# Kernel tuning notes

Hardware: AMD Instinct MI355X
Metric: run time of the kernel (lower is better)

## Reference

```python
import jax, jax.numpy as jnp
import numpy as np

NBITS = 4
GROUP = 128
K = 4096   # in_features
N = 4096   # out_features
M = 4096   # flattened batch*seq tokens
EPS = 32 // NBITS  # elements per packed int32 = 8
MASK = (1 << NBITS) - 1  # unpack_mask = 15


def setup_inputs() -> dict:
    key = jax.random.key(0)
    k1, k2, k3, k4, k5 = jax.random.split(key, 5)
    x = jax.random.normal(k1, (M, K), dtype=jnp.float32)
    # raw 4-bit quantized weights, layout [K, N] (i.e. W_q.t() from the torch module)
    nib = jax.random.randint(k2, (K, N), 0, 1 << NBITS, dtype=jnp.int32)
    # pack EPS nibbles per int32 along K, matching pack(): element j gets shift j*NBITS
    nib = nib.reshape(K // EPS, EPS, N)
    shifts = (jnp.arange(EPS, dtype=jnp.int32) * NBITS)[None, :, None]
    parts = nib << shifts  # disjoint bit ranges
    W_q_packed = parts[:, 0]
    for j in range(1, EPS):
        W_q_packed = W_q_packed | parts[:, j]
    W_q_packed = W_q_packed.astype(jnp.int32)  # [K//EPS, N]
    # group-wise scales/zeros: [K//GROUP, N] (scales.view(N,-1).t() layout)
    scales = (jax.random.uniform(k3, (K // GROUP, N), dtype=jnp.float32) + 0.5) * 0.01
    zeros = jax.random.uniform(k4, (K // GROUP, N), dtype=jnp.float32) * MASK
    bias = jax.random.normal(k5, (N,), dtype=jnp.float32) * 0.1
    return {"x": x, "W_q_packed": W_q_packed, "scales": scales, "zeros": zeros, "bias": bias}


def reference(x, W_q_packed, scales, zeros, bias):
    # unpack: w[k, n] = (packed[k//EPS, n] >> ((k % EPS) * NBITS)) & MASK
    shifts = (jnp.arange(EPS, dtype=jnp.int32) * NBITS)[None, :, None]
    w = (W_q_packed[:, None, :] >> shifts) & MASK  # [K//EPS, EPS, N]
    w = w.reshape(K, N).astype(jnp.float32)
    # group-wise asymmetric dequant (W_group_mode == 3): W = (w - z) * s
    s = jnp.repeat(scales, GROUP, axis=0)  # [K, N]
    z = jnp.repeat(zeros, GROUP, axis=0)   # [K, N]
    W = (w - z) * s
    out = x @ W + bias  # [M, N]
    return out
```

## Files before the change

kernel.cpp:

```cpp
#include <hip/hip_runtime.h>
#include <stdint.h>


#define M_DIM 4096
#define N_DIM 4096
#define K_DIM 4096
#define NT (K_DIM / 64)

typedef __attribute__((ext_vector_type(8))) short short8;
typedef __attribute__((ext_vector_type(4))) float f32x4;

__device__ __forceinline__ unsigned short f2bf(float f) {
  uint32_t u = __builtin_bit_cast(uint32_t, f);
  u += 0x7fffu + ((u >> 16) & 1u);
  return (unsigned short)(u >> 16);
}

__global__ __launch_bounds__(256) void prep_kernel(const float* __restrict__ x,
                                                   unsigned short* __restrict__ xb,
                                                   const int* __restrict__ Wq,
                                                   const float* __restrict__ scales,
                                                   const float* __restrict__ zeros,
                                                   unsigned short* __restrict__ wt) {
  __shared__ uint4 Ts[32 * 64];
  const int tid = threadIdx.x;
  if (blockIdx.x < 2048) {
    const int total = (M_DIM * K_DIM) / 8;
    const float4* x4 = (const float4*)x;
    uint4* o8 = (uint4*)xb;
#pragma unroll
    for (int p = 0; p < 4; ++p) {
      int i = (p * 2048 + blockIdx.x) * 256 + tid;
      if (i < total) {
        float4 a = x4[2 * i], b = x4[2 * i + 1];
        uint4 o;
        o.x = (uint32_t)f2bf(a.x) | ((uint32_t)f2bf(a.y) << 16);
        o.y = (uint32_t)f2bf(a.z) | ((uint32_t)f2bf(a.w) << 16);
        o.z = (uint32_t)f2bf(b.x) | ((uint32_t)f2bf(b.y) << 16);
        o.w = (uint32_t)f2bf(b.z) | ((uint32_t)f2bf(b.w) << 16);
        o8[i] = o;
      }
    }
    return;
  }
  const int blk = blockIdx.x - 2048;
  const int n0 = (blk & 127) * 32;
  const int gk0 = (blk >> 7) * 64;

#pragma unroll
  for (int p = 0; p < 8; ++p) {
    int e = p * 256 + tid;
    int n_l = e & 31;
    int gk_l = e >> 5;
    int gk = gk0 + gk_l;
    int n = n0 + n_l;
    int g = gk >> 4;
    uint32_t q = (uint32_t)Wq[gk * N_DIM + n];
    float s = scales[g * N_DIM + n];
    float z = zeros[g * N_DIM + n];
    unsigned short b[8];
#pragma unroll
    for (int j = 0; j < 8; ++j) {
      float f = ((float)((q >> (4 * j)) & 15u) - z) * s;
      b[j] = f2bf(f);
    }
    uint4 cell;
    cell.x = (uint32_t)b[0] | ((uint32_t)b[1] << 16);
    cell.y = (uint32_t)b[2] | ((uint32_t)b[3] << 16);
    cell.z = (uint32_t)b[4] | ((uint32_t)b[5] << 16);
    cell.w = (uint32_t)b[6] | ((uint32_t)b[7] << 16);
    Ts[n_l * 64 + (gk_l ^ (n_l & 7))] = cell;
  }
  __syncthreads();
  uint4* dst = (uint4*)wt;
#pragma unroll
  for (int p = 0; p < 8; ++p) {
    int n_l = p * 4 + (tid >> 6);
    int gk_l = tid & 63;
    uint4 cell = Ts[n_l * 64 + (gk_l ^ (n_l & 7))];
    dst[(size_t)(n0 + n_l) * (K_DIM / 8) + (gk0 + gk_l)] = cell;
  }
}


#define STAGE4(DST, SRC)                                                         \
  {                                                                              \
    _Pragma("unroll") for (int j = 0; j < 4; ++j)                                \
        __builtin_amdgcn_global_load_lds(                                        \
            (const __attribute__((address_space(1))) void*)((SRC) +              \
                                                            (size_t)j * 64 * K_DIM), \
            (__attribute__((address_space(3))) void*)((DST) + tid + j * 512),    \
            16, 0, 0);                                                           \
  }

#define LOADA(QM)                                                                \
  {                                                                              \
    _Pragma("unroll") for (int mi = 0; mi < 4; ++mi) {                           \
      af[mi][0] = ASb[a_base + ((QM) * 4 + mi) * 128 + kx0];                     \
      af[mi][1] = ASb[a_base + ((QM) * 4 + mi) * 128 + kx1];                     \
    }                                                                            \
  }

#define LOADBALL                                                                 \
  {                                                                              \
    _Pragma("unroll") for (int nn = 0; nn < 4; ++nn) {                           \
      bv[nn][0] = BSb[b_base + nn * 128 + kx0];                                  \
      bv[nn][1] = BSb[b_base + nn * 128 + kx1];                                  \
    }                                                                            \
  }

#define MFMA16(QM, QN)                                                           \
  {                                                                              \
    __builtin_amdgcn_s_setprio(1);                                               \
    _Pragma("unroll") for (int mi = 0; mi < 4; ++mi)                             \
        _Pragma("unroll") for (int ni = 0; ni < 2; ++ni) {                       \
      acc[(QM) * 4 + mi][(QN) * 2 + ni] = __builtin_amdgcn_mfma_f32_16x16x32_bf16( \
          af[mi][0], bv[(QN) * 2 + ni][0], acc[(QM) * 4 + mi][(QN) * 2 + ni], 0, 0, 0); \
      acc[(QM) * 4 + mi][(QN) * 2 + ni] = __builtin_amdgcn_mfma_f32_16x16x32_bf16( \
          af[mi][1], bv[(QN) * 2 + ni][1], acc[(QM) * 4 + mi][(QN) * 2 + ni], 0, 0, 0); \
    }                                                                            \
    __builtin_amdgcn_s_setprio(0);                                               \
  }

__global__ __launch_bounds__(512, 2) void gemm_bt_kernel(
    const unsigned short* __restrict__ A, const unsigned short* __restrict__ Bt,
    const float* __restrict__ bias, float* __restrict__ C) {
  __shared__ short8 As[2 * 2048];
  __shared__ short8 Bs[2 * 2048];

  const int tid = threadIdx.x;
  const int lane = tid & 63;
  const int w = tid >> 6;
  const int wm = w >> 2;
  const int wn = w & 3;

  const int b = blockIdx.x;
  const int xcd = b & 7;
  const int loc = b >> 3;
  const int nt = xcd * 2 + (loc & 1);
  const int mt = loc >> 1;
  const int m0 = mt * 256;
  const int n0 = nt * 256;

  const int srow = tid >> 3;
  const int skc = (tid & 7) ^ (srow & 7);
  const unsigned short* Ablk = A + (size_t)m0 * K_DIM + (size_t)srow * K_DIM + skc * 8;
  const unsigned short* Bblk = Bt + (size_t)n0 * K_DIM + (size_t)srow * K_DIM + skc * 8;

  const int fr = lane & 15;
  const int fc = lane >> 4;
  const int frx = fr & 7;
  const int a_base = (wm * 128 + fr) * 8;
  const int b_base = (wn * 64 + fr) * 8;
  const int kx0 = fc ^ frx;
  const int kx1 = (4 + fc) ^ frx;

  f32x4 acc[8][4] = {};
  short8 af[4][2];
  short8 bv[4][2];

  STAGE4(As, Ablk);
  STAGE4(Bs, Bblk);
  STAGE4(As + 2048, Ablk + 64);
  STAGE4(Bs + 2048, Bblk + 64);
  asm volatile("s_waitcnt vmcnt(8)" ::: "memory");
  __builtin_amdgcn_sched_barrier(0);
  __builtin_amdgcn_s_barrier();

  for (int kt = 0; kt < NT; ++kt) {
    const int cur = kt & 1;
    const short8* ASb = As + cur * 2048;
    const short8* BSb = Bs + cur * 2048;

    LOADA(0);
    LOADBALL;
    MFMA16(0, 0);
    MFMA16(0, 1);
    LOADA(1);
    MFMA16(1, 1);
    MFMA16(1, 0);

    asm volatile("s_waitcnt lgkmcnt(0)" ::: "memory");
    __builtin_amdgcn_sched_barrier(0);
    __builtin_amdgcn_s_barrier();
    if (kt + 2 < NT) {
      STAGE4(As + cur * 2048, Ablk + (size_t)(kt + 2) * 64);
      STAGE4(Bs + cur * 2048, Bblk + (size_t)(kt + 2) * 64);
      asm volatile("s_waitcnt vmcnt(8)" ::: "memory");
    } else {
      asm volatile("s_waitcnt vmcnt(0)" ::: "memory");
    }
    __builtin_amdgcn_sched_barrier(0);
    __builtin_amdgcn_s_barrier();
  }

  const int rr = (lane >> 4) * 4;
#pragma unroll
  for (int ni = 0; ni < 4; ++ni) {
    const int gn = n0 + wn * 64 + ni * 16 + fr;
    const float bvv = bias[gn];
#pragma unroll
    for (int mi = 0; mi < 8; ++mi) {
      const int gm = m0 + wm * 128 + mi * 16 + rr;
#pragma unroll
      for (int r = 0; r < 4; ++r)
        C[(size_t)(gm + r) * N_DIM + gn] = acc[mi][ni][r] + bvv;
    }
  }
}

extern "C" void kernel_launch(void* const* d_in, const int* in_sizes, int n_in,
                              void* d_out, int out_size, void* d_ws, size_t ws_size,
                              hipStream_t stream) {
  const float* x = (const float*)d_in[0];
  const int* wq = (const int*)d_in[1];
  const float* sc = (const float*)d_in[2];
  const float* zr = (const float*)d_in[3];
  const float* bias = (const float*)d_in[4];
  float* out = (float*)d_out;

  unsigned short* xb = (unsigned short*)d_ws;
  unsigned short* wt = (unsigned short*)((char*)d_ws + (size_t)M_DIM * K_DIM * 2);

  prep_kernel<<<dim3(3072), dim3(256), 0, stream>>>(x, xb, wq, sc, zr, wt);
  gemm_bt_kernel<<<dim3(256), dim3(512), 0, stream>>>(xb, wt, bias, out);
}
```

Before: 269.6 us.

## Split GEMM main loop into four half-tile phases with finer-grained prefetch

The 256x256 block tile is now split into 128-row and 128-column halves, and each wave's fragment ownership is remapped so that every wave covers two row halves and two column halves. The K-step is broken into four phases. Each phase loads only the fragments it needs, issues half-tile global-to-LDS prefetches (next stage for the second halves, stage k+2 for the first halves), and waits on partial vmcnt. The aim is to overlap global loads with MFMA more evenly and cut register pressure for B fragments. In exchange it adds more barriers per iteration and more complex wait counting, which could stall or race.

```diff
diff --git a/kernel.cpp b/kernel.cpp
--- a/kernel.cpp
+++ b/kernel.cpp
@@ -83,44 +83,52 @@
 }
 
 
-#define STAGE4(DST, SRC)                                                         \
-  {                                                                              \
-    _Pragma("unroll") for (int j = 0; j < 4; ++j)                                \
-        __builtin_amdgcn_global_load_lds(                                        \
-            (const __attribute__((address_space(1))) void*)((SRC) +              \
-                                                            (size_t)j * 64 * K_DIM), \
-            (__attribute__((address_space(3))) void*)((DST) + tid + j * 512),    \
-            16, 0, 0);                                                           \
-  }
-
-#define LOADA(QM)                                                                \
-  {                                                                              \
-    _Pragma("unroll") for (int mi = 0; mi < 4; ++mi) {                           \
-      af[mi][0] = ASb[a_base + ((QM) * 4 + mi) * 128 + kx0];                     \
-      af[mi][1] = ASb[a_base + ((QM) * 4 + mi) * 128 + kx1];                     \
-    }                                                                            \
-  }
-
-#define LOADBALL                                                                 \
-  {                                                                              \
-    _Pragma("unroll") for (int nn = 0; nn < 4; ++nn) {                           \
-      bv[nn][0] = BSb[b_base + nn * 128 + kx0];                                  \
-      bv[nn][1] = BSb[b_base + nn * 128 + kx1];                                  \
-    }                                                                            \
-  }
-
-#define MFMA16(QM, QN)                                                           \
-  {                                                                              \
-    __builtin_amdgcn_s_setprio(1);                                               \
-    _Pragma("unroll") for (int mi = 0; mi < 4; ++mi)                             \
-        _Pragma("unroll") for (int ni = 0; ni < 2; ++ni) {                       \
-      acc[(QM) * 4 + mi][(QN) * 2 + ni] = __builtin_amdgcn_mfma_f32_16x16x32_bf16( \
-          af[mi][0], bv[(QN) * 2 + ni][0], acc[(QM) * 4 + mi][(QN) * 2 + ni], 0, 0, 0); \
-      acc[(QM) * 4 + mi][(QN) * 2 + ni] = __builtin_amdgcn_mfma_f32_16x16x32_bf16( \
-          af[mi][1], bv[(QN) * 2 + ni][1], acc[(QM) * 4 + mi][(QN) * 2 + ni], 0, 0, 0); \
-    }                                                                            \
-    __builtin_amdgcn_s_setprio(0);                                               \
-  }
+#define STAGEH(DST, SRC)                                                        \
+  {                                                                             \
+    __builtin_amdgcn_global_load_lds(                                           \
+        (const __attribute__((address_space(1))) void*)(SRC),                   \
+        (__attribute__((address_space(3))) void*)((DST) + tid), 16, 0, 0);      \
+    __builtin_amdgcn_global_load_lds(                                           \
+        (const __attribute__((address_space(1))) void*)((SRC) + 64 * K_DIM),    \
+        (__attribute__((address_space(3))) void*)((DST) + tid + 512), 16, 0, 0);\
+  }
+
+#define LOADAF(RB)                                                              \
+  {                                                                             \
+    _Pragma("unroll") for (int mi = 0; mi < 4; ++mi) {                          \
+      af[mi][0] = ASb[(RB)*1024 + a_base + mi * 128 + kx0];                     \
+      af[mi][1] = ASb[(RB)*1024 + a_base + mi * 128 + kx1];                     \
+    }                                                                           \
+  }
+
+#define LOADBV(CB)                                                              \
+  {                                                                             \
+    _Pragma("unroll") for (int ni = 0; ni < 2; ++ni) {                          \
+      bv[ni][0] = BSb[(CB)*1024 + b_base + ni * 128 + kx0];                     \
+      bv[ni][1] = BSb[(CB)*1024 + b_base + ni * 128 + kx1];                     \
+    }                                                                           \
+  }
+
+#define MFMAQ(RB, CB)                                                           \
+  {                                                                             \
+    __builtin_amdgcn_s_setprio(1);                                              \
+    _Pragma("unroll") for (int mi = 0; mi < 4; ++mi)                            \
+        _Pragma("unroll") for (int ni = 0; ni < 2; ++ni) {                      \
+      acc[(RB)*4 + mi][(CB)*2 + ni] = __builtin_amdgcn_mfma_f32_16x16x32_bf16(  \
+          af[mi][0], bv[ni][0], acc[(RB)*4 + mi][(CB)*2 + ni], 0, 0, 0);        \
+      acc[(RB)*4 + mi][(CB)*2 + ni] = __builtin_amdgcn_mfma_f32_16x16x32_bf16(  \
+          af[mi][1], bv[ni][1], acc[(RB)*4 + mi][(CB)*2 + ni], 0, 0, 0);        \
+    }                                                                           \
+    __builtin_amdgcn_s_setprio(0);                                              \
+  }
+
+#define WAIT_VM6                                           \
+  asm volatile("s_waitcnt vmcnt(6)" ::: "memory");         \
+  __builtin_amdgcn_sched_barrier(0);
+
+#define WAIT_LGKM0                                         \
+  asm volatile("s_waitcnt lgkmcnt(0)" ::: "memory");       \
+  __builtin_amdgcn_sched_barrier(0);
 
 __global__ __launch_bounds__(512, 2) void gemm_bt_kernel(
     const unsigned short* __restrict__ A, const unsigned short* __restrict__ Bt,
@@ -144,25 +152,29 @@
 
   const int srow = tid >> 3;
   const int skc = (tid & 7) ^ (srow & 7);
-  const unsigned short* Ablk = A + (size_t)m0 * K_DIM + (size_t)srow * K_DIM + skc * 8;
-  const unsigned short* Bblk = Bt + (size_t)n0 * K_DIM + (size_t)srow * K_DIM + skc * 8;
+  const unsigned short* Asrc0 = A + (size_t)(m0 + srow) * K_DIM + skc * 8;
+  const unsigned short* Asrc1 = Asrc0 + (size_t)128 * K_DIM;
+  const unsigned short* Bsrc0 = Bt + (size_t)(n0 + srow) * K_DIM + skc * 8;
+  const unsigned short* Bsrc1 = Bsrc0 + (size_t)128 * K_DIM;
 
   const int fr = lane & 15;
   const int fc = lane >> 4;
   const int frx = fr & 7;
-  const int a_base = (wm * 128 + fr) * 8;
-  const int b_base = (wn * 64 + fr) * 8;
+  const int a_base = (wm * 64 + fr) * 8;
+  const int b_base = (wn * 32 + fr) * 8;
   const int kx0 = fc ^ frx;
   const int kx1 = (4 + fc) ^ frx;
 
   f32x4 acc[8][4] = {};
   short8 af[4][2];
-  short8 bv[4][2];
-
-  STAGE4(As, Ablk);
-  STAGE4(Bs, Bblk);
-  STAGE4(As + 2048, Ablk + 64);
-  STAGE4(Bs + 2048, Bblk + 64);
+  short8 bv[2][2];
+
+  STAGEH(As, Asrc0);
+  STAGEH(Bs, Bsrc0);
+  STAGEH(Bs + 1024, Bsrc1);
+  STAGEH(As + 1024, Asrc1);
+  STAGEH(As + 2048, Asrc0 + 64);
+  STAGEH(Bs + 2048, Bsrc0 + 64);
   asm volatile("s_waitcnt vmcnt(8)" ::: "memory");
   __builtin_amdgcn_sched_barrier(0);
   __builtin_amdgcn_s_barrier();
@@ -171,42 +183,65 @@
     const int cur = kt & 1;
     const short8* ASb = As + cur * 2048;
     const short8* BSb = Bs + cur * 2048;
-
-    LOADA(0);
-    LOADBALL;
-    MFMA16(0, 0);
-    MFMA16(0, 1);
-    LOADA(1);
-    MFMA16(1, 1);
-    MFMA16(1, 0);
-
-    asm volatile("s_waitcnt lgkmcnt(0)" ::: "memory");
-    __builtin_amdgcn_sched_barrier(0);
-    __builtin_amdgcn_s_barrier();
-    if (kt + 2 < NT) {
-      STAGE4(As + cur * 2048, Ablk + (size_t)(kt + 2) * 64);
-      STAGE4(Bs + cur * 2048, Bblk + (size_t)(kt + 2) * 64);
-      asm volatile("s_waitcnt vmcnt(8)" ::: "memory");
-    } else {
-      asm volatile("s_waitcnt vmcnt(0)" ::: "memory");
+    short8* Anx = As + (cur ^ 1) * 2048;
+    short8* Bnx = Bs + (cur ^ 1) * 2048;
+    short8* Asame = As + cur * 2048;
+    short8* Bsame = Bs + cur * 2048;
+    const bool p1ok = (kt + 1 < NT);
+    const bool p2ok = (kt + 2 < NT);
+
+    WAIT_VM6;
+    LOADAF(0);
+    LOADBV(0);
+    if (p1ok) STAGEH(Bnx + 1024, Bsrc1 + (size_t)(kt + 1) * 64);
+    __builtin_amdgcn_s_barrier();
+    WAIT_LGKM0;
+    MFMAQ(0, 0);
+    __builtin_amdgcn_s_barrier();
+
+    WAIT_VM6;
+    LOADBV(1);
+    if (p1ok) STAGEH(Anx + 1024, Asrc1 + (size_t)(kt + 1) * 64);
+    __builtin_amdgcn_s_barrier();
+    WAIT_LGKM0;
+    MFMAQ(0, 1);
+    __builtin_amdgcn_s_barrier();
+
+    WAIT_VM6;
+    LOADAF(1);
+    LOADBV(0);
+    if (p2ok) STAGEH(Asame, Asrc0 + (size_t)(kt + 2) * 64);
+    __builtin_amdgcn_s_barrier();
+    WAIT_LGKM0;
+    MFMAQ(1, 0);
+    __builtin_amdgcn_s_barrier();
+
+    WAIT_VM6;
+    LOADBV(1);
+    if (p2ok) STAGEH(Bsame, Bsrc0 + (size_t)(kt + 2) * 64);
+    __builtin_amdgcn_s_barrier();
+    WAIT_LGKM0;
+    MFMAQ(1, 1);
+    __builtin_amdgcn_s_barrier();
+  }
+
+  const int rr = (lane >> 4) * 4;
+#pragma unroll
+  for (int cb = 0; cb < 2; ++cb)
+#pragma unroll
+    for (int ni = 0; ni < 2; ++ni) {
+      const int gn = n0 + cb * 128 + wn * 32 + ni * 16 + fr;
+      const float bvv = bias[gn];
+#pragma unroll
+      for (int rb = 0; rb < 2; ++rb)
+#pragma unroll
+        for (int mi = 0; mi < 4; ++mi) {
+          const int gm = m0 + rb * 128 + wm * 64 + mi * 16 + rr;
+#pragma unroll
+          for (int r = 0; r < 4; ++r)
+            C[(size_t)(gm + r) * N_DIM + gn] = acc[rb * 4 + mi][cb * 2 + ni][r] + bvv;
+        }
     }
-    __builtin_amdgcn_sched_barrier(0);
-    __builtin_amdgcn_s_barrier();
-  }
-
-  const int rr = (lane >> 4) * 4;
-#pragma unroll
-  for (int ni = 0; ni < 4; ++ni) {
-    const int gn = n0 + wn * 64 + ni * 16 + fr;
-    const float bvv = bias[gn];
-#pragma unroll
-    for (int mi = 0; mi < 8; ++mi) {
-      const int gm = m0 + wm * 128 + mi * 16 + rr;
-#pragma unroll
-      for (int r = 0; r < 4; ++r)
-        C[(size_t)(gm + r) * N_DIM + gn] = acc[mi][ni][r] + bvv;
-    }
-  }
 }
 
 extern "C" void kernel_launch(void* const* d_in, const int* in_sizes, int n_in,
```

New measurement: 262.9 us. -2.5%, faster.
